# Performance work log

Hardware: AMD Instinct MI355X
Metric: run time of the kernel (lower is better)

Reference implementation:

```python
import jax, jax.numpy as jnp
import numpy as np

N_NODES = 100000
N_FEAT = 128
HIDDEN = 32
HEADS = 4
N_CLASSES = 40
N_EDGES = 1600000
NEG_SLOPE = 0.2


def gat_conv(x, src, dst, W, att_src, att_dst, bias):
    """PyG-style GATConv (concat=True, eval mode, self-loops already in src/dst).
    x: [N, Fin], W: [Fin, H*C], att_src/att_dst: [H, C], bias: [H*C].
    """
    N = x.shape[0]
    H, C = att_src.shape
    h = (x @ W).reshape(N, H, C)                       # [N, H, C]
    a_src = jnp.einsum('nhc,hc->nh', h, att_src)       # [N, H]
    a_dst = jnp.einsum('nhc,hc->nh', h, att_dst)       # [N, H]
    e = a_src[src] + a_dst[dst]                        # [E, H]
    e = jnp.where(e > 0, e, NEG_SLOPE * e)             # leaky_relu(0.2)
    # segment softmax over incoming edges of each destination node
    e_max = jax.ops.segment_max(e, dst, num_segments=N)
    e = jnp.exp(e - e_max[dst])
    denom = jax.ops.segment_sum(e, dst, num_segments=N)
    alpha = e / (denom[dst] + 1e-16)                   # [E, H]
    msg = alpha[:, :, None] * h[src]                   # [E, H, C]
    out = jax.ops.segment_sum(msg, dst, num_segments=N)  # [N, H, C]
    return out.reshape(N, H * C) + bias


def setup_inputs() -> dict:
    key = jax.random.key(0)
    ks = jax.random.split(key, 10)
    s = 0.1
    x = jax.random.normal(ks[0], (N_NODES, N_FEAT), dtype=jnp.float32)
    edge_index = jax.random.randint(ks[1], (2, N_EDGES), 0, N_NODES, dtype=jnp.int32)
    W1 = jax.random.normal(ks[2], (N_FEAT, HEADS * HIDDEN), dtype=jnp.float32) * s
    att_src1 = jax.random.normal(ks[3], (HEADS, HIDDEN), dtype=jnp.float32) * s
    att_dst1 = jax.random.normal(ks[4], (HEADS, HIDDEN), dtype=jnp.float32) * s
    b1 = jnp.zeros((HEADS * HIDDEN,), dtype=jnp.float32)
    W2 = jax.random.normal(ks[5], (HEADS * HIDDEN, HEADS * HIDDEN), dtype=jnp.float32) * s
    att_src2 = jax.random.normal(ks[6], (HEADS, HIDDEN), dtype=jnp.float32) * s
    att_dst2 = jax.random.normal(ks[7], (HEADS, HIDDEN), dtype=jnp.float32) * s
    b2 = jnp.zeros((HEADS * HIDDEN,), dtype=jnp.float32)
    Wc = jax.random.normal(ks[8], (HEADS * HIDDEN, N_CLASSES), dtype=jnp.float32) * s
    bc = jnp.zeros((N_CLASSES,), dtype=jnp.float32)
    return {"x": x, "edge_index": edge_index, "W1": W1, "att_src1": att_src1,
            "att_dst1": att_dst1, "b1": b1, "W2": W2, "att_src2": att_src2,
            "att_dst2": att_dst2, "b2": b2, "Wc": Wc, "bc": bc}


def reference(x, edge_index, W1, att_src1, att_dst1, b1, W2, att_src2, att_dst2, b2, Wc, bc):
    N = x.shape[0]
    loops = jnp.arange(N, dtype=edge_index.dtype)
    src = jnp.concatenate([edge_index[0], loops])  # PyG add_self_loops=True
    dst = jnp.concatenate([edge_index[1], loops])
    h = gat_conv(x, src, dst, W1, att_src1, att_dst1, b1)
    h = jax.nn.relu(h)  # dropout p=0.5 inactive in eval
    h = gat_conv(h, src, dst, W2, att_src2, att_dst2, b2)
    h = jax.nn.relu(h)  # dropout p=0.6 inactive in eval
    return h @ Wc + bc
```

## Files before the change

kernel.cpp:

```cpp
#include <hip/hip_runtime.h>

#define NN   100000
#define NE   1600000
#define BSH  9
#define BSZ  512
#define NBK  196
#define TA   8192
#define NBA  196
#define CAP  8704
#define CAP2 9216
#define NBG  782
#define NPREP 6

typedef _Float16 half_t;
typedef __attribute__((ext_vector_type(2))) _Float16 f16x2;
typedef __attribute__((ext_vector_type(4))) _Float16 f16x4;
typedef __attribute__((ext_vector_type(8))) _Float16 f16x8;
typedef __attribute__((ext_vector_type(4))) float    f32x4;

__global__ __launch_bounds__(256) void k_front(const float* __restrict__ X, const float* __restrict__ W1,
                                               const float* __restrict__ atts, const float* __restrict__ attd,
                                               half_t* __restrict__ H, float* __restrict__ asrc,
                                               float* __restrict__ adst,
                                               const float* __restrict__ W2, const float* __restrict__ Wc,
                                               half_t* __restrict__ WT2, half_t* __restrict__ WTc,
                                               int* __restrict__ bcur) {
  __shared__ __align__(16) char smem[20480];
  int t = threadIdx.x;
  int bid = blockIdx.x;

  if (bid == NBG + NPREP) {
    if (t < NBK) bcur[t] = t * CAP;
    return;
  }

  if (bid >= NBG) {
    int b = bid - NBG;
    float (*tile)[65] = (float(*)[65])smem;
    const float* W;
    half_t* WT;
    int k0, n0, N, NTr;
    if (b < 4) { W = W2; WT = WT2; k0 = (b >> 1) * 64; n0 = (b & 1) * 64; N = 128; NTr = 128; }
    else       { int bb = b - 4; W = Wc; WT = WTc; k0 = bb * 64; n0 = 0; N = 40; NTr = 48; }
    int col = t & 63, r4 = t >> 6;
#pragma unroll
    for (int i = 0; i < 16; i++) {
      int row = r4 * 16 + i;
      float v = 0.f;
      if (n0 + col < N) v = W[(size_t)(k0 + row) * N + n0 + col];
      tile[row][col] = v;
    }
    __syncthreads();
#pragma unroll
    for (int i = 0; i < 16; i++) {
      int nrow = r4 * 16 + i;
      if (n0 + nrow < NTr) WT[(size_t)(n0 + nrow) * 128 + k0 + col] = (half_t)tile[col][nrow];
    }
    return;
  }

  half_t* Xt = (half_t*)smem;
  half_t* Wt = Xt + 128 * 40;
  int wave = t >> 6, lane = t & 63;
  int l15 = lane & 15, quad = lane >> 4;
  int rb = bid * 128;

  f32x4 acc[2][8];
#pragma unroll
  for (int rt = 0; rt < 2; rt++)
#pragma unroll
    for (int ct = 0; ct < 8; ct++) acc[rt][ct] = (f32x4){0.f, 0.f, 0.f, 0.f};

  for (int k0 = 0; k0 < 128; k0 += 32) {
    __syncthreads();
#pragma unroll
    for (int i = 0; i < 4; i++) {
      int lin = i * 256 + t;
      int row = lin >> 3;
      int c4 = (lin & 7) * 4;
      float4 v = make_float4(0.f, 0.f, 0.f, 0.f);
      int gr = rb + row;
      if (gr < NN) v = *(const float4*)(X + (size_t)gr * 128 + k0 + c4);
      f16x4 hv;
      hv[0] = (half_t)v.x; hv[1] = (half_t)v.y; hv[2] = (half_t)v.z; hv[3] = (half_t)v.w;
      *(f16x4*)(Xt + row * 40 + c4) = hv;
    }
#pragma unroll
    for (int i = 0; i < 4; i++) {
      int lin = i * 256 + t;
      int kr = lin >> 5;
      int n4 = (lin & 31) * 4;
      float4 v = *(const float4*)(W1 + (size_t)(k0 + kr) * 128 + n4);
      Wt[(n4 + 0) * 40 + kr] = (half_t)v.x;
      Wt[(n4 + 1) * 40 + kr] = (half_t)v.y;
      Wt[(n4 + 2) * 40 + kr] = (half_t)v.z;
      Wt[(n4 + 3) * 40 + kr] = (half_t)v.w;
    }
    __syncthreads();

    f16x8 a0 = *(const f16x8*)(Xt + (wave * 32 + l15) * 40 + quad * 8);
    f16x8 a1 = *(const f16x8*)(Xt + (wave * 32 + 16 + l15) * 40 + quad * 8);
#pragma unroll
    for (int ct = 0; ct < 8; ct++) {
      f16x8 b = *(const f16x8*)(Wt + (ct * 16 + l15) * 40 + quad * 8);
      acc[0][ct] = __builtin_amdgcn_mfma_f32_16x16x32_f16(a0, b, acc[0][ct], 0, 0, 0);
      acc[1][ct] = __builtin_amdgcn_mfma_f32_16x16x32_f16(a1, b, acc[1][ct], 0, 0, 0);
    }
  }

#pragma unroll
  for (int rt = 0; rt < 2; rt++) {
    int rbase = rb + wave * 32 + rt * 16 + quad * 4;
#pragma unroll
    for (int reg = 0; reg < 4; reg++) {
      int row = rbase + reg;
      if (row < NN) {
#pragma unroll
        for (int ct = 0; ct < 8; ct++) {
          H[(size_t)row * 128 + ct * 16 + l15] = (half_t)acc[rt][ct][reg];
        }
      }
    }
  }

  float s_lo[4], s_hi[4], d_lo[4], d_hi[4];
#pragma unroll
  for (int h = 0; h < 4; h++) {
    s_lo[h] = atts[h * 32 + l15];
    s_hi[h] = atts[h * 32 + 16 + l15];
    d_lo[h] = attd[h * 32 + l15];
    d_hi[h] = attd[h * 32 + 16 + l15];
  }
#pragma unroll
  for (int rt = 0; rt < 2; rt++) {
    float ps[4][4], pd[4][4];
#pragma unroll
    for (int reg = 0; reg < 4; reg++)
#pragma unroll
      for (int h = 0; h < 4; h++) {
        ps[reg][h] = acc[rt][2 * h][reg] * s_lo[h] + acc[rt][2 * h + 1][reg] * s_hi[h];
        pd[reg][h] = acc[rt][2 * h][reg] * d_lo[h] + acc[rt][2 * h + 1][reg] * d_hi[h];
      }
#pragma unroll
    for (int m = 1; m < 16; m <<= 1) {
#pragma unroll
      for (int reg = 0; reg < 4; reg++)
#pragma unroll
        for (int h = 0; h < 4; h++) {
          ps[reg][h] += __shfl_xor(ps[reg][h], m, 64);
          pd[reg][h] += __shfl_xor(pd[reg][h], m, 64);
        }
    }
    float vs = 0.f, vd = 0.f;
#pragma unroll
    for (int reg = 0; reg < 4; reg++)
#pragma unroll
      for (int h = 0; h < 4; h++) {
        if (l15 == reg * 4 + h) { vs = ps[reg][h]; vd = pd[reg][h]; }
      }
    int row = rb + wave * 32 + rt * 16 + quad * 4 + (l15 >> 2);
    int h = l15 & 3;
    if (row < NN) {
      asrc[row * 4 + h] = vs;
      adst[row * 4 + h] = vd;
    }
  }
}

__global__ __launch_bounds__(256) void k_binA(const int* __restrict__ src, const int* __restrict__ dst,
                                              int* __restrict__ bcur, unsigned int* __restrict__ bpk) {
  __shared__ int hist[NBK];
  __shared__ int hscan[NBK];
  __shared__ int gbase[NBK];
  __shared__ int cnt[NBK];
  __shared__ int ssc[256];
  __shared__ unsigned int staged[TA];
  int t = threadIdx.x;
  int e0 = blockIdx.x * TA;
  if (t < NBK) { hist[t] = 0; cnt[t] = 0; }
  __syncthreads();
#pragma unroll
  for (int i = 0; i < TA / 256; i++) {
    int e = e0 + t + i * 256;
    if (e < NE) atomicAdd(&hist[dst[e] >> BSH], 1);
  }
  __syncthreads();
  {
    int v = (t < NBK) ? hist[t] : 0;
    int x = v;
    ssc[t] = x;
    for (int off = 1; off < 256; off <<= 1) {
      __syncthreads();
      int y = (t >= off) ? ssc[t - off] : 0;
      __syncthreads();
      x += y;
      ssc[t] = x;
    }
    if (t < NBK) {
      hscan[t] = x - v;
      if (v > 0) gbase[t] = atomicAdd(&bcur[t], v);
    }
  }
  __syncthreads();
#pragma unroll
  for (int i = 0; i < TA / 256; i++) {
    int e = e0 + t + i * 256;
    if (e < NE) {
      int d = dst[e];
      int b = d >> BSH;
      int pos = hscan[b] + atomicAdd(&cnt[b], 1);
      staged[pos] = ((unsigned int)src[e] << BSH) | (unsigned int)(d & (BSZ - 1));
    }
  }
  __syncthreads();
  int wave = t >> 6, lane = t & 63;
  for (int b = wave; b < NBK; b += 4) {
    int c = hist[b];
    if (c > 0) {
      int lo = hscan[b], gb = gbase[b];
      for (int j = lane; j < c; j += 64) bpk[gb + j] = staged[lo + j];
    }
  }
}

__global__ __launch_bounds__(256) void k_binB(const unsigned int* __restrict__ bpk,
                                              const int* __restrict__ bcur,
                                              int* __restrict__ sbeg, int* __restrict__ send,
                                              int* __restrict__ adj) {
  __shared__ int lhist[BSZ];
  __shared__ int lscan[BSZ];
  __shared__ int lcur[BSZ];
  __shared__ int ssc[256];
  __shared__ unsigned int staged[CAP2];
  int b = blockIdx.x;
  int t = threadIdx.x;
  int nbeg = b << BSH;
  int nloc = min(BSZ, NN - nbeg);
  int ebeg = b * CAP;
  int ecnt = bcur[b] - ebeg;
  int adjb = b * CAP2;
  int total = ecnt + nloc;
  lhist[2 * t] = (2 * t < nloc) ? 1 : 0;
  lhist[2 * t + 1] = (2 * t + 1 < nloc) ? 1 : 0;
  lcur[2 * t] = 1;
  lcur[2 * t + 1] = 1;
  __syncthreads();
  for (int i = t; i < ecnt; i += 256) atomicAdd(&lhist[bpk[ebeg + i] & (BSZ - 1)], 1);
  __syncthreads();
  {
    int v0 = lhist[2 * t], v1 = lhist[2 * t + 1];
    int s2 = v0 + v1;
    int x = s2;
    ssc[t] = x;
    for (int off = 1; off < 256; off <<= 1) {
      __syncthreads();
      int y = (t >= off) ? ssc[t - off] : 0;
      __syncthreads();
      x += y;
      ssc[t] = x;
    }
    int ex = x - s2;
    lscan[2 * t] = ex;
    lscan[2 * t + 1] = ex + v0;
  }
  __syncthreads();
#pragma unroll
  for (int u = 0; u < 2; u++) {
    int i = t + u * 256;
    if (i < nloc) {
      int bg = adjb + lscan[i];
      sbeg[nbeg + i] = bg;
      send[nbeg + i] = bg + lhist[i];
      staged[lscan[i]] = (unsigned int)(nbeg + i);
    }
  }
  __syncthreads();
  for (int i = t; i < ecnt; i += 256) {
    unsigned int v = bpk[ebeg + i];
    int dl = v & (BSZ - 1);
    int idx = lscan[dl] + atomicAdd(&lcur[dl], 1);
    staged[idx] = v >> BSH;
  }
  __syncthreads();
  for (int i = t; i < total; i += 256) adj[adjb + i] = (int)staged[i];
}

__global__ __launch_bounds__(256) void k_agg(const half_t* __restrict__ H, const int* __restrict__ sbeg,
                                             const int* __restrict__ send, const int* __restrict__ adj,
                                             const float* __restrict__ asrc, const float* __restrict__ adst,
                                             const float* __restrict__ bias, half_t* __restrict__ out) {
  int n = blockIdx.x * 4 + (threadIdx.x >> 6);
  if (n >= NN) return;
  int lane = threadIdx.x & 63;
  int l15 = lane & 15, g = lane >> 4;
  int head = l15 >> 2;
  float ad = adst[(size_t)n * 4 + head];
  float acc[8] = {0.f, 0.f, 0.f, 0.f, 0.f, 0.f, 0.f, 0.f};
  float wsum = 0.f;
  int beg = sbeg[n], end = send[n];
  int i = beg + g;
  int s = 0;
  float a = 0.f;
  if (i < end) {
    s = adj[i];
    a = asrc[(size_t)s * 4 + head];
  }
  while (i < end) {
    int inext = i + 4;
    int sn = 0;
    float an = 0.f;
    if (inext < end) {
      sn = adj[inext];
      an = asrc[(size_t)sn * 4 + head];
    }
    float ev = a + ad;
    ev = (ev > 0.f) ? ev : 0.2f * ev;
    float w = __expf(ev);
    f16x8 hv = *(const f16x8*)(H + (size_t)s * 128 + l15 * 8);
    wsum += w;
#pragma unroll
    for (int j = 0; j < 8; j++) acc[j] += w * (float)hv[j];
    s = sn; a = an; i = inext;
  }
#pragma unroll
  for (int m = 16; m < 64; m <<= 1) {
    wsum += __shfl_xor(wsum, m, 64);
#pragma unroll
    for (int j = 0; j < 8; j++) acc[j] += __shfl_xor(acc[j], m, 64);
  }
  float scale = 1.0f / (wsum + 1e-16f);
  float o0 = acc[0], o1 = acc[1];
  if (g == 1) { o0 = acc[2]; o1 = acc[3]; }
  if (g == 2) { o0 = acc[4]; o1 = acc[5]; }
  if (g == 3) { o0 = acc[6]; o1 = acc[7]; }
  int ch = l15 * 8 + g * 2;
  o0 = fmaxf(o0 * scale + bias[ch], 0.f);
  o1 = fmaxf(o1 * scale + bias[ch + 1], 0.f);
  f16x2 o;
  o[0] = (half_t)o0;
  o[1] = (half_t)o1;
  *(f16x2*)(out + (size_t)n * 128 + ch) = o;
}

__global__ __launch_bounds__(256) void k_gemm_att(const half_t* __restrict__ X, const half_t* __restrict__ WT,
                                                  const float* __restrict__ atts, const float* __restrict__ attd,
                                                  half_t* __restrict__ H, float* __restrict__ asrc,
                                                  float* __restrict__ adst) {
  __shared__ __align__(16) half_t Xt[128 * 40];
  __shared__ __align__(16) half_t Wt[128 * 40];
  int t = threadIdx.x;
  int wave = t >> 6, lane = t & 63;
  int l15 = lane & 15, quad = lane >> 4;
  int rb = blockIdx.x * 128;

  f32x4 acc[2][8];
#pragma unroll
  for (int rt = 0; rt < 2; rt++)
#pragma unroll
    for (int ct = 0; ct < 8; ct++) acc[rt][ct] = (f32x4){0.f, 0.f, 0.f, 0.f};

  for (int k0 = 0; k0 < 128; k0 += 32) {
    __syncthreads();
#pragma unroll
    for (int i = 0; i < 2; i++) {
      int lin = i * 256 + t;
      int row = lin >> 2;
      int c8 = (lin & 3) * 8;
      f16x8 hv = (f16x8)(half_t)0;
      int gr = rb + row;
      if (gr < NN) hv = *(const f16x8*)(X + (size_t)gr * 128 + k0 + c8);
      *(f16x8*)(Xt + row * 40 + c8) = hv;
    }
#pragma unroll
    for (int i = 0; i < 2; i++) {
      int lin = i * 256 + t;
      int row = lin >> 2;
      int c8 = (lin & 3) * 8;
      *(f16x8*)(Wt + row * 40 + c8) = *(const f16x8*)(WT + (size_t)row * 128 + k0 + c8);
    }
    __syncthreads();

    f16x8 a0 = *(const f16x8*)(Xt + (wave * 32 + l15) * 40 + quad * 8);
    f16x8 a1 = *(const f16x8*)(Xt + (wave * 32 + 16 + l15) * 40 + quad * 8);
#pragma unroll
    for (int ct = 0; ct < 8; ct++) {
      f16x8 b = *(const f16x8*)(Wt + (ct * 16 + l15) * 40 + quad * 8);
      acc[0][ct] = __builtin_amdgcn_mfma_f32_16x16x32_f16(a0, b, acc[0][ct], 0, 0, 0);
      acc[1][ct] = __builtin_amdgcn_mfma_f32_16x16x32_f16(a1, b, acc[1][ct], 0, 0, 0);
    }
  }

#pragma unroll
  for (int rt = 0; rt < 2; rt++) {
    int rbase = rb + wave * 32 + rt * 16 + quad * 4;
#pragma unroll
    for (int reg = 0; reg < 4; reg++) {
      int row = rbase + reg;
      if (row < NN) {
#pragma unroll
        for (int ct = 0; ct < 8; ct++) {
          H[(size_t)row * 128 + ct * 16 + l15] = (half_t)acc[rt][ct][reg];
        }
      }
    }
  }

  float s_lo[4], s_hi[4], d_lo[4], d_hi[4];
#pragma unroll
  for (int h = 0; h < 4; h++) {
    s_lo[h] = atts[h * 32 + l15];
    s_hi[h] = atts[h * 32 + 16 + l15];
    d_lo[h] = attd[h * 32 + l15];
    d_hi[h] = attd[h * 32 + 16 + l15];
  }
#pragma unroll
  for (int rt = 0; rt < 2; rt++) {
    float ps[4][4], pd[4][4];
#pragma unroll
    for (int reg = 0; reg < 4; reg++)
#pragma unroll
      for (int h = 0; h < 4; h++) {
        ps[reg][h] = acc[rt][2 * h][reg] * s_lo[h] + acc[rt][2 * h + 1][reg] * s_hi[h];
        pd[reg][h] = acc[rt][2 * h][reg] * d_lo[h] + acc[rt][2 * h + 1][reg] * d_hi[h];
      }
#pragma unroll
    for (int m = 1; m < 16; m <<= 1) {
#pragma unroll
      for (int reg = 0; reg < 4; reg++)
#pragma unroll
        for (int h = 0; h < 4; h++) {
          ps[reg][h] += __shfl_xor(ps[reg][h], m, 64);
          pd[reg][h] += __shfl_xor(pd[reg][h], m, 64);
        }
    }
    float vs = 0.f, vd = 0.f;
#pragma unroll
    for (int reg = 0; reg < 4; reg++)
#pragma unroll
      for (int h = 0; h < 4; h++) {
        if (l15 == reg * 4 + h) { vs = ps[reg][h]; vd = pd[reg][h]; }
      }
    int row = rb + wave * 32 + rt * 16 + quad * 4 + (l15 >> 2);
    int h = l15 & 3;
    if (row < NN) {
      asrc[row * 4 + h] = vs;
      adst[row * 4 + h] = vd;
    }
  }
}

__global__ __launch_bounds__(256) void k_classifier(const half_t* __restrict__ Hf, const half_t* __restrict__ WTc,
                                                    const float* __restrict__ bc, float* __restrict__ out) {
  __shared__ __align__(16) half_t Xt[128 * 40];
  __shared__ __align__(16) half_t Wt[48 * 40];
  int t = threadIdx.x;
  int wave = t >> 6, lane = t & 63;
  int l15 = lane & 15, quad = lane >> 4;
  int rb = blockIdx.x * 128;

  f32x4 acc[2][3];
#pragma unroll
  for (int rt = 0; rt < 2; rt++)
#pragma unroll
    for (int ct = 0; ct < 3; ct++) acc[rt][ct] = (f32x4){0.f, 0.f, 0.f, 0.f};

  for (int k0 = 0; k0 < 128; k0 += 32) {
    __syncthreads();
#pragma unroll
    for (int i = 0; i < 2; i++) {
      int lin = i * 256 + t;
      int row = lin >> 2;
      int c8 = (lin & 3) * 8;
      f16x8 hv = (f16x8)(half_t)0;
      int gr = rb + row;
      if (gr < NN) hv = *(const f16x8*)(Hf + (size_t)gr * 128 + k0 + c8);
      *(f16x8*)(Xt + row * 40 + c8) = hv;
    }
    if (t < 192) {
      int row = t >> 2;
      int c8 = (t & 3) * 8;
      *(f16x8*)(Wt + row * 40 + c8) = *(const f16x8*)(WTc + (size_t)row * 128 + k0 + c8);
    }
    __syncthreads();

    f16x8 a0 = *(const f16x8*)(Xt + (wave * 32 + l15) * 40 + quad * 8);
    f16x8 a1 = *(const f16x8*)(Xt + (wave * 32 + 16 + l15) * 40 + quad * 8);
#pragma unroll
    for (int ct = 0; ct < 3; ct++) {
      f16x8 b = *(const f16x8*)(Wt + (ct * 16 + l15) * 40 + quad * 8);
      acc[0][ct] = __builtin_amdgcn_mfma_f32_16x16x32_f16(a0, b, acc[0][ct], 0, 0, 0);
      acc[1][ct] = __builtin_amdgcn_mfma_f32_16x16x32_f16(a1, b, acc[1][ct], 0, 0, 0);
    }
  }

#pragma unroll
  for (int rt = 0; rt < 2; rt++) {
#pragma unroll
    for (int ct = 0; ct < 3; ct++) {
      int col = ct * 16 + l15;
      if (col < 40) {
        float bv = bc[col];
#pragma unroll
        for (int reg = 0; reg < 4; reg++) {
          int row = rb + wave * 32 + rt * 16 + quad * 4 + reg;
          if (row < NN) out[(size_t)row * 40 + col] = acc[rt][ct][reg] + bv;
        }
      }
    }
  }
}


extern "C" void kernel_launch(void* const* d_in, const int* in_sizes, int n_in,
                              void* d_out, int out_size, void* d_ws, size_t ws_size,
                              hipStream_t stream) {
  const float* x   = (const float*)d_in[0];
  const int*   ei  = (const int*)d_in[1];
  const float* W1  = (const float*)d_in[2];
  const float* as1 = (const float*)d_in[3];
  const float* ad1 = (const float*)d_in[4];
  const float* b1  = (const float*)d_in[5];
  const float* W2  = (const float*)d_in[6];
  const float* as2 = (const float*)d_in[7];
  const float* ad2 = (const float*)d_in[8];
  const float* b2  = (const float*)d_in[9];
  const float* Wc  = (const float*)d_in[10];
  const float* bc  = (const float*)d_in[11];
  float* out = (float*)d_out;

  const int* esrc = ei;
  const int* edst = ei + NE;

  char* w = (char*)d_ws;
  auto alloc = [&](size_t bytes) {
    void* p = (void*)w;
    w += (bytes + 255) & ~(size_t)255;
    return p;
  };
  half_t* A   = (half_t*)alloc(sizeof(half_t) * (size_t)NN * 128);
  half_t* B   = (half_t*)alloc(sizeof(half_t) * (size_t)NN * 128);
  float* asrc = (float*)alloc(sizeof(float) * (size_t)NN * 4);
  float* adst = (float*)alloc(sizeof(float) * (size_t)NN * 4);
  int* sbeg   = (int*)alloc(sizeof(int) * NN);
  int* send   = (int*)alloc(sizeof(int) * NN);
  unsigned int* bpk = (unsigned int*)alloc(sizeof(unsigned int) * (size_t)NBK * CAP);
  int* adj    = (int*)alloc(sizeof(int) * (size_t)NBK * CAP2);
  half_t* WT2 = (half_t*)alloc(sizeof(half_t) * 128 * 128);
  half_t* WTc = (half_t*)alloc(sizeof(half_t) * 48 * 128);
  int* bcur   = (int*)alloc(sizeof(int) * NBK);

  k_front<<<NBG + NPREP + 1, 256, 0, stream>>>(x, W1, as1, ad1, A, asrc, adst,
                                               W2, Wc, WT2, WTc, bcur);
  k_binA<<<NBA, 256, 0, stream>>>(esrc, edst, bcur, bpk);
  k_binB<<<NBK, 256, 0, stream>>>(bpk, bcur, sbeg, send, adj);

  k_agg<<<(NN + 3) / 4, 256, 0, stream>>>(A, sbeg, send, adj, asrc, adst, b1, B);

  k_gemm_att<<<(NN + 127) / 128, 256, 0, stream>>>(B, WT2, as2, ad2, A, asrc, adst);
  k_agg<<<(NN + 3) / 4, 256, 0, stream>>>(A, sbeg, send, adj, asrc, adst, b2, B);

  k_classifier<<<(NN + 127) / 128, 256, 0, stream>>>(B, WTc, bc, out);
}
```

Baseline: 414.7 us.

## Fuse edge binning into front kernel with fixed slots; widen aggregation edge parallelism

```diff
diff --git a/kernel.cpp b/kernel.cpp
--- a/kernel.cpp
+++ b/kernel.cpp
@@ -7,7 +7,7 @@
 #define NBK  196
 #define TA   8192
 #define NBA  196
-#define CAP  8704
+#define SCAP 96
 #define CAP2 9216
 #define NBG  782
 #define NPREP 6
@@ -24,13 +24,62 @@
                                                float* __restrict__ adst,
                                                const float* __restrict__ W2, const float* __restrict__ Wc,
                                                half_t* __restrict__ WT2, half_t* __restrict__ WTc,
-                                               int* __restrict__ bcur) {
-  __shared__ __align__(16) char smem[20480];
+                                               const int* __restrict__ src, const int* __restrict__ dst,
+                                               unsigned int* __restrict__ bpk, int* __restrict__ bh) {
+  __shared__ __align__(16) char smem[36864];
   int t = threadIdx.x;
   int bid = blockIdx.x;
 
-  if (bid == NBG + NPREP) {
-    if (t < NBK) bcur[t] = t * CAP;
+  if (bid >= NBG + NPREP) {
+    int hb = bid - NBG - NPREP;
+    int* hist  = (int*)smem;
+    int* hscan = hist + NBK;
+    int* cnt   = hscan + NBK;
+    int* ssc   = cnt + NBK;
+    unsigned int* staged = (unsigned int*)(ssc + 256);
+    int e0 = hb * TA;
+    if (t < NBK) { hist[t] = 0; cnt[t] = 0; }
+    __syncthreads();
+#pragma unroll
+    for (int i = 0; i < TA / 256; i++) {
+      int e = e0 + t + i * 256;
+      if (e < NE) atomicAdd(&hist[dst[e] >> BSH], 1);
+    }
+    __syncthreads();
+    {
+      int v = (t < NBK) ? hist[t] : 0;
+      int x = v;
+      ssc[t] = x;
+      for (int off = 1; off < 256; off <<= 1) {
+        __syncthreads();
+        int y = (t >= off) ? ssc[t - off] : 0;
+        __syncthreads();
+        x += y;
+        ssc[t] = x;
+      }
+      if (t < NBK) hscan[t] = x - v;
+    }
+    __syncthreads();
+#pragma unroll
+    for (int i = 0; i < TA / 256; i++) {
+      int e = e0 + t + i * 256;
+      if (e < NE) {
+        int d = dst[e];
+        int bk = d >> BSH;
+        int pos = hscan[bk] + atomicAdd(&cnt[bk], 1);
+        staged[pos] = ((unsigned int)src[e] << BSH) | (unsigned int)(d & (BSZ - 1));
+      }
+    }
+    __syncthreads();
+    int wave = t >> 6, lane = t & 63;
+    for (int bk = wave; bk < NBK; bk += 4) {
+      int c = hist[bk];
+      int cw = min(c, SCAP);
+      size_t base = ((size_t)bk * NBA + hb) * SCAP;
+      int lo = hscan[bk];
+      for (int j = lane; j < cw; j += 64) bpk[base + j] = staged[lo + j];
+      if (lane == 0) bh[bk * NBA + hb] = cw;
+    }
     return;
   }
 
@@ -167,85 +216,33 @@
   }
 }
 
-__global__ __launch_bounds__(256) void k_binA(const int* __restrict__ src, const int* __restrict__ dst,
-                                              int* __restrict__ bcur, unsigned int* __restrict__ bpk) {
-  __shared__ int hist[NBK];
-  __shared__ int hscan[NBK];
-  __shared__ int gbase[NBK];
-  __shared__ int cnt[NBK];
-  __shared__ int ssc[256];
-  __shared__ unsigned int staged[TA];
-  int t = threadIdx.x;
-  int e0 = blockIdx.x * TA;
-  if (t < NBK) { hist[t] = 0; cnt[t] = 0; }
-  __syncthreads();
-#pragma unroll
-  for (int i = 0; i < TA / 256; i++) {
-    int e = e0 + t + i * 256;
-    if (e < NE) atomicAdd(&hist[dst[e] >> BSH], 1);
-  }
-  __syncthreads();
-  {
-    int v = (t < NBK) ? hist[t] : 0;
-    int x = v;
-    ssc[t] = x;
-    for (int off = 1; off < 256; off <<= 1) {
-      __syncthreads();
-      int y = (t >= off) ? ssc[t - off] : 0;
-      __syncthreads();
-      x += y;
-      ssc[t] = x;
-    }
-    if (t < NBK) {
-      hscan[t] = x - v;
-      if (v > 0) gbase[t] = atomicAdd(&bcur[t], v);
-    }
-  }
-  __syncthreads();
-#pragma unroll
-  for (int i = 0; i < TA / 256; i++) {
-    int e = e0 + t + i * 256;
-    if (e < NE) {
-      int d = dst[e];
-      int b = d >> BSH;
-      int pos = hscan[b] + atomicAdd(&cnt[b], 1);
-      staged[pos] = ((unsigned int)src[e] << BSH) | (unsigned int)(d & (BSZ - 1));
-    }
-  }
-  __syncthreads();
-  int wave = t >> 6, lane = t & 63;
-  for (int b = wave; b < NBK; b += 4) {
-    int c = hist[b];
-    if (c > 0) {
-      int lo = hscan[b], gb = gbase[b];
-      for (int j = lane; j < c; j += 64) bpk[gb + j] = staged[lo + j];
-    }
-  }
-}
-
 __global__ __launch_bounds__(256) void k_binB(const unsigned int* __restrict__ bpk,
-                                              const int* __restrict__ bcur,
+                                              const int* __restrict__ bh,
                                               int* __restrict__ sbeg, int* __restrict__ send,
                                               int* __restrict__ adj) {
   __shared__ int lhist[BSZ];
   __shared__ int lscan[BSZ];
   __shared__ int lcur[BSZ];
   __shared__ int ssc[256];
+  __shared__ int carr[NBA];
   __shared__ unsigned int staged[CAP2];
   int b = blockIdx.x;
   int t = threadIdx.x;
   int nbeg = b << BSH;
   int nloc = min(BSZ, NN - nbeg);
-  int ebeg = b * CAP;
-  int ecnt = bcur[b] - ebeg;
   int adjb = b * CAP2;
-  int total = ecnt + nloc;
+  if (t < NBA) carr[t] = bh[b * NBA + t];
   lhist[2 * t] = (2 * t < nloc) ? 1 : 0;
   lhist[2 * t + 1] = (2 * t + 1 < nloc) ? 1 : 0;
   lcur[2 * t] = 1;
   lcur[2 * t + 1] = 1;
   __syncthreads();
-  for (int i = t; i < ecnt; i += 256) atomicAdd(&lhist[bpk[ebeg + i] & (BSZ - 1)], 1);
+  int wave = t >> 6, lane = t & 63;
+  for (int a = wave; a < NBA; a += 4) {
+    int c = carr[a];
+    size_t base = ((size_t)b * NBA + a) * SCAP;
+    for (int j = lane; j < c; j += 64) atomicAdd(&lhist[bpk[base + j] & (BSZ - 1)], 1);
+  }
   __syncthreads();
   {
     int v0 = lhist[2 * t], v1 = lhist[2 * t + 1];
@@ -264,6 +261,7 @@
     lscan[2 * t + 1] = ex + v0;
   }
   __syncthreads();
+  int total = lscan[BSZ - 1] + lhist[BSZ - 1];
 #pragma unroll
   for (int u = 0; u < 2; u++) {
     int i = t + u * 256;
@@ -275,14 +273,19 @@
     }
   }
   __syncthreads();
-  for (int i = t; i < ecnt; i += 256) {
-    unsigned int v = bpk[ebeg + i];
-    int dl = v & (BSZ - 1);
-    int idx = lscan[dl] + atomicAdd(&lcur[dl], 1);
-    staged[idx] = v >> BSH;
+  for (int a = wave; a < NBA; a += 4) {
+    int c = carr[a];
+    size_t base = ((size_t)b * NBA + a) * SCAP;
+    for (int j = lane; j < c; j += 64) {
+      unsigned int v = bpk[base + j];
+      int dl = v & (BSZ - 1);
+      int idx = lscan[dl] + atomicAdd(&lcur[dl], 1);
+      if (idx < CAP2) staged[idx] = v >> BSH;
+    }
   }
   __syncthreads();
-  for (int i = t; i < total; i += 256) adj[adjb + i] = (int)staged[i];
+  int lim = min(total, CAP2);
+  for (int i = t; i < lim; i += 256) adj[adjb + i] = (int)staged[i];
 }
 
 __global__ __launch_bounds__(256) void k_agg(const half_t* __restrict__ H, const int* __restrict__ sbeg,
@@ -292,10 +295,13 @@
   int n = blockIdx.x * 4 + (threadIdx.x >> 6);
   if (n >= NN) return;
   int lane = threadIdx.x & 63;
-  int l15 = lane & 15, g = lane >> 4;
-  int head = l15 >> 2;
+  int sub = lane & 7;
+  int g = lane >> 3;
+  int head = sub >> 1;
   float ad = adst[(size_t)n * 4 + head];
-  float acc[8] = {0.f, 0.f, 0.f, 0.f, 0.f, 0.f, 0.f, 0.f};
+  float acc[16];
+#pragma unroll
+  for (int j = 0; j < 16; j++) acc[j] = 0.f;
   float wsum = 0.f;
   int beg = sbeg[n], end = send[n];
   int i = beg + g;
@@ -306,7 +312,7 @@
     a = asrc[(size_t)s * 4 + head];
   }
   while (i < end) {
-    int inext = i + 4;
+    int inext = i + 8;
     int sn = 0;
     float an = 0.f;
     if (inext < end) {
@@ -316,24 +322,28 @@
     float ev = a + ad;
     ev = (ev > 0.f) ? ev : 0.2f * ev;
     float w = __expf(ev);
-    f16x8 hv = *(const f16x8*)(H + (size_t)s * 128 + l15 * 8);
+    const f16x8* hp = (const f16x8*)(H + (size_t)s * 128 + sub * 16);
+    f16x8 h0 = hp[0], h1 = hp[1];
     wsum += w;
 #pragma unroll
-    for (int j = 0; j < 8; j++) acc[j] += w * (float)hv[j];
+    for (int j = 0; j < 8; j++) acc[j] += w * (float)h0[j];
+#pragma unroll
+    for (int j = 0; j < 8; j++) acc[8 + j] += w * (float)h1[j];
     s = sn; a = an; i = inext;
   }
 #pragma unroll
-  for (int m = 16; m < 64; m <<= 1) {
+  for (int m = 8; m < 64; m <<= 1) {
     wsum += __shfl_xor(wsum, m, 64);
 #pragma unroll
-    for (int j = 0; j < 8; j++) acc[j] += __shfl_xor(acc[j], m, 64);
+    for (int j = 0; j < 16; j++) acc[j] += __shfl_xor(acc[j], m, 64);
   }
   float scale = 1.0f / (wsum + 1e-16f);
   float o0 = acc[0], o1 = acc[1];
-  if (g == 1) { o0 = acc[2]; o1 = acc[3]; }
-  if (g == 2) { o0 = acc[4]; o1 = acc[5]; }
-  if (g == 3) { o0 = acc[6]; o1 = acc[7]; }
-  int ch = l15 * 8 + g * 2;
+#pragma unroll
+  for (int r = 1; r < 8; r++) {
+    if (g == r) { o0 = acc[2 * r]; o1 = acc[2 * r + 1]; }
+  }
+  int ch = sub * 16 + g * 2;
   o0 = fmaxf(o0 * scale + bias[ch], 0.f);
   o1 = fmaxf(o1 * scale + bias[ch + 1], 0.f);
   f16x2 o;
@@ -543,16 +553,15 @@
   float* adst = (float*)alloc(sizeof(float) * (size_t)NN * 4);
   int* sbeg   = (int*)alloc(sizeof(int) * NN);
   int* send   = (int*)alloc(sizeof(int) * NN);
-  unsigned int* bpk = (unsigned int*)alloc(sizeof(unsigned int) * (size_t)NBK * CAP);
+  unsigned int* bpk = (unsigned int*)alloc(sizeof(unsigned int) * (size_t)NBK * NBA * SCAP);
+  int* bh     = (int*)alloc(sizeof(int) * NBK * NBA);
   int* adj    = (int*)alloc(sizeof(int) * (size_t)NBK * CAP2);
   half_t* WT2 = (half_t*)alloc(sizeof(half_t) * 128 * 128);
   half_t* WTc = (half_t*)alloc(sizeof(half_t) * 48 * 128);
-  int* bcur   = (int*)alloc(sizeof(int) * NBK);
-
-  k_front<<<NBG + NPREP + 1, 256, 0, stream>>>(x, W1, as1, ad1, A, asrc, adst,
-                                               W2, Wc, WT2, WTc, bcur);
-  k_binA<<<NBA, 256, 0, stream>>>(esrc, edst, bcur, bpk);
-  k_binB<<<NBK, 256, 0, stream>>>(bpk, bcur, sbeg, send, adj);
+
+  k_front<<<NBG + NPREP + NBA, 256, 0, stream>>>(x, W1, as1, ad1, A, asrc, adst,
+                                                 W2, Wc, WT2, WTc, esrc, edst, bpk, bh);
+  k_binB<<<NBK, 256, 0, stream>>>(bpk, bh, sbeg, send, adj);
 
   k_agg<<<(NN + 3) / 4, 256, 0, stream>>>(A, sbeg, send, adj, asrc, adst, b1, B);
 
```

Measured after the change: 400.8 us. -3.3%, faster.
